# Optimization experiments

Measured on AMD Instinct MI355X. Metric: run time of the kernel, lower is better.

Reference implementation:

```python
import jax, jax.numpy as jnp
import numpy as np

FEATURE_DIM = 128
NUM_EDGES = 640000
NUM_NODES = 40000


def setup_inputs() -> dict:
    key = jax.random.key(0)
    ks = jax.random.split(key, 10)
    d = FEATURE_DIM
    scale = 1.0 / np.sqrt(d)
    inp = {
        "messages": jax.random.normal(ks[0], (NUM_EDGES, d), dtype=jnp.float32),
        "receivers": jax.random.randint(ks[1], (NUM_EDGES,), 0, NUM_NODES, dtype=jnp.int32),
        "num_segments": NUM_NODES,
        "Wk": jax.random.normal(ks[2], (d, d), dtype=jnp.float32) * scale,
        "bk": jnp.zeros((d,), dtype=jnp.float32),
        "Wv": jax.random.normal(ks[3], (d, d), dtype=jnp.float32) * scale,
        "bv": jnp.zeros((d,), dtype=jnp.float32),
        "Wq": jax.random.normal(ks[4], (d, d), dtype=jnp.float32) * scale,
        "bq": jnp.zeros((d,), dtype=jnp.float32),
        "Wo": jax.random.normal(ks[5], (d, d), dtype=jnp.float32) * scale,
        "bo": jnp.zeros((d,), dtype=jnp.float32),
    }
    return inp


def reference(messages, receivers, num_segments, Wk, bk, Wv, bv, Wq, bq, Wo, bo):
    d = messages.shape[-1]
    # per-edge key/value projections
    keys = messages @ Wk + bk            # [E, d]
    values = messages @ Wv + bv          # [E, d]
    # node-level summed messages -> queries
    summed = jax.ops.segment_sum(messages, receivers, num_segments)  # [N, d]
    queries = summed @ Wq + bq                                       # [N, d]
    # scalar attention score per edge (dot over full feature dim)
    msg_q = queries[receivers]                                       # [E, d]
    scores = jnp.sum(msg_q * keys, axis=-1) / jnp.sqrt(jnp.float32(d))  # [E]
    # segment softmax over edges sharing a receiver
    max_s = jax.ops.segment_max(scores, receivers, num_segments)     # [N]
    exp_s = jnp.exp(scores - max_s[receivers])                       # [E]
    sum_e = jax.ops.segment_sum(exp_s, receivers, num_segments)      # [N]
    attn = exp_s / (sum_e[receivers] + 1e-08)                        # [E]
    # weighted scatter-sum of values, then output projection
    agg = jax.ops.segment_sum(values * attn[:, None], receivers, num_segments)  # [N, d]
    return agg @ Wo + bo
```

## Files before the change

### kernel.cpp

```cpp
#include <hip/hip_runtime.h>
#include <hip/hip_bf16.h>

#define D 128
#define RSQRT_D 0.088388347648318440550f


__global__ void hist_kernel(const int* __restrict__ recv, int* __restrict__ cnt, int E) {
    int e = blockIdx.x * blockDim.x + threadIdx.x;
    if (e >= E) return;
    atomicAdd(&cnt[recv[e]], 1);
}

#define SCAN_B 256
__global__ void scan1_kernel(const int* __restrict__ cnt, int* __restrict__ excl,
                             int* __restrict__ bsum, int N) {
    __shared__ int tmp[SCAN_B];
    int i = blockIdx.x * SCAN_B + threadIdx.x;
    int v = (i < N) ? cnt[i] : 0;
    tmp[threadIdx.x] = v;
    __syncthreads();
#pragma unroll
    for (int off = 1; off < SCAN_B; off <<= 1) {
        int t = (threadIdx.x >= off) ? tmp[threadIdx.x - off] : 0;
        __syncthreads();
        tmp[threadIdx.x] += t;
        __syncthreads();
    }
    if (i < N) excl[i] = tmp[threadIdx.x] - v;
    if (threadIdx.x == SCAN_B - 1) bsum[blockIdx.x] = tmp[threadIdx.x];
}

__global__ void scan2_kernel(int* __restrict__ bsum, int nb) {
    __shared__ int tmp[SCAN_B];
    int v = (threadIdx.x < nb) ? bsum[threadIdx.x] : 0;
    tmp[threadIdx.x] = v;
    __syncthreads();
#pragma unroll
    for (int off = 1; off < SCAN_B; off <<= 1) {
        int t = (threadIdx.x >= off) ? tmp[threadIdx.x - off] : 0;
        __syncthreads();
        tmp[threadIdx.x] += t;
        __syncthreads();
    }
    if (threadIdx.x < nb) bsum[threadIdx.x] = tmp[threadIdx.x] - v;
}

__global__ void scan3_kernel(const int* __restrict__ excl, const int* __restrict__ bsum,
                             int* __restrict__ start, int N, int E) {
    int i = blockIdx.x * SCAN_B + threadIdx.x;
    if (i < N) start[i] = excl[i] + bsum[blockIdx.x];
    if (i == N) start[N] = E;
}

__global__ void fill_kernel(const int* __restrict__ recv, const int* __restrict__ start,
                            int* __restrict__ cursor, int* __restrict__ eidx, int E) {
    int e = blockIdx.x * blockDim.x + threadIdx.x;
    if (e >= E) return;
    int r = recv[e];
    int p = atomicAdd(&cursor[r], 1);
    eidx[start[r] + p] = e;
}


__global__ void fold_wvo_kernel(const float* __restrict__ Wv, const float* __restrict__ Wo,
                                const float* __restrict__ bv,
                                float* __restrict__ Wvo, float* __restrict__ bvo) {
    int j = threadIdx.x;
    int i = blockIdx.x;
    if (i < D) {
        float acc = 0.f;
        for (int k = 0; k < D; ++k) acc += Wv[(size_t)i * D + k] * Wo[(size_t)k * D + j];
        Wvo[(size_t)i * D + j] = acc;
    } else {
        float acc = 0.f;
        for (int k = 0; k < D; ++k) acc += bv[k] * Wo[(size_t)k * D + j];
        bvo[j] = acc;
    }
}

__global__ void fold_wqk_kernel(const float* __restrict__ Wq, const float* __restrict__ Wk,
                                const float* __restrict__ bq, const float* __restrict__ bk,
                                float* __restrict__ Wqk, float* __restrict__ bqk,
                                float* __restrict__ wqb, float* __restrict__ bqb) {
    int j = threadIdx.x;
    int i = blockIdx.x;
    if (i < D) {
        float acc = 0.f;
        for (int t = 0; t < D; ++t) acc += Wq[(size_t)i * D + t] * Wk[(size_t)j * D + t];
        Wqk[(size_t)i * D + j] = acc;
    } else if (i == D) {
        float acc = 0.f;
        for (int t = 0; t < D; ++t) acc += bq[t] * Wk[(size_t)j * D + t];
        bqk[j] = acc;
    } else {
        float acc = 0.f;
        for (int t = 0; t < D; ++t) acc += Wq[(size_t)j * D + t] * bk[t];
        wqb[j] = acc;
        if (j == 0) {
            float b = 0.f;
            for (int t = 0; t < D; ++t) b += bq[t] * bk[t];
            *bqb = b;
        }
    }
}


__global__ __launch_bounds__(256) void nodesum_kernel(
        const float* __restrict__ msg, const int* __restrict__ eidx,
        const int* __restrict__ start, float* __restrict__ summed, int N) {
    int wave = threadIdx.x >> 6;
    int lane = threadIdx.x & 63;
    int n = blockIdx.x * 4 + wave;
    if (n >= N) return;
    int s0 = start[n], s1 = start[n + 1];
    float2 acc = make_float2(0.f, 0.f);
    for (int j = s0; j < s1; ++j) {
        int e = eidx[j];
        float2 mm = ((const float2*)(msg + (size_t)e * D))[lane];
        acc.x += mm.x;
        acc.y += mm.y;
    }
    ((float2*)(summed + (size_t)n * D))[lane] = acc;
}

__global__ __launch_bounds__(256) void attn_kernel(
        const float* __restrict__ msg, const int* __restrict__ eidx,
        const int* __restrict__ start, const float* __restrict__ qk,
        const float* __restrict__ qb, float* __restrict__ S,
        float* __restrict__ sumexp, int N) {
    int wave = threadIdx.x >> 6;
    int lane = threadIdx.x & 63;
    int n = blockIdx.x * 4 + wave;
    if (n >= N) return;
    int s0 = start[n], s1 = start[n + 1];
    float2 q = ((const float2*)(qk + (size_t)n * D))[lane];
    float qbn = qb[n];
    float m = -3.4e38f, ssum = 0.f;
    float2 acc = make_float2(0.f, 0.f);

    float2 cur;
    if (s0 < s1) {
        int e0 = eidx[s0];
        cur = ((const float2*)(msg + (size_t)e0 * D))[lane];
    }
    for (int j = s0; j < s1; ++j) {
        float2 nxt;
        if (j + 1 < s1) {
            int e1 = eidx[j + 1];
            nxt = ((const float2*)(msg + (size_t)e1 * D))[lane];
        }
        float p = cur.x * q.x + cur.y * q.y;
#pragma unroll
        for (int off = 1; off < 64; off <<= 1) p += __shfl_xor(p, off);
        float sc = (p + qbn) * RSQRT_D;
        float nm = fmaxf(m, sc);
        float scale = __expf(m - nm);
        float ee = __expf(sc - nm);
        ssum = ssum * scale + ee;
        acc.x = acc.x * scale + ee * cur.x;
        acc.y = acc.y * scale + ee * cur.y;
        m = nm;
        cur = nxt;
    }
    float w = 1.f / (ssum + 1e-8f);
    ((float2*)(S + (size_t)n * D))[lane] = make_float2(acc.x * w, acc.y * w);
    if (lane == 0) sumexp[n] = ssum;
}


#define GN 32
__global__ __launch_bounds__(256) void gemm128_kernel(
        const float* __restrict__ A, const float* __restrict__ B,
        float* __restrict__ C,
        const float* __restrict__ bias,
        const float* __restrict__ sumexp,
        const float* __restrict__ bvec,
        int N) {
    __shared__ float Bs[D * D];
    __shared__ float As[GN * D];
    int t = threadIdx.x;
    const float4* Bg4 = (const float4*)B;
    float4* Bs4 = (float4*)Bs;
#pragma unroll
    for (int k = 0; k < 16; ++k) Bs4[t + 256 * k] = Bg4[t + 256 * k];
    int n0 = blockIdx.x * GN;
    const float4* Ag4 = (const float4*)(A + (size_t)n0 * D);
    float4* As4 = (float4*)As;
#pragma unroll
    for (int k = 0; k < 4; ++k) As4[t + 256 * k] = Ag4[t + 256 * k];
    __syncthreads();

    int c = t & 31;
    int slot = t >> 5;
    float4 acc[4];
#pragma unroll
    for (int u = 0; u < 4; ++u) acc[u] = make_float4(0.f, 0.f, 0.f, 0.f);
    const float4* Bsr = (const float4*)Bs;
    for (int i = 0; i < D; i += 4) {
        float4 a[4];
#pragma unroll
        for (int u = 0; u < 4; ++u) a[u] = *(const float4*)(As + (slot + 8 * u) * D + i);
#pragma unroll
        for (int ii = 0; ii < 4; ++ii) {
            float4 b = Bsr[(i + ii) * 32 + c];
#pragma unroll
            for (int u = 0; u < 4; ++u) {
                float av = (ii == 0) ? a[u].x : (ii == 1) ? a[u].y : (ii == 2) ? a[u].z : a[u].w;
                acc[u].x += av * b.x; acc[u].y += av * b.y;
                acc[u].z += av * b.z; acc[u].w += av * b.w;
            }
        }
    }
    float4 bias4 = bias ? ((const float4*)bias)[c] : make_float4(0.f, 0.f, 0.f, 0.f);
    float4 bv4 = bvec ? ((const float4*)bvec)[c] : make_float4(0.f, 0.f, 0.f, 0.f);
#pragma unroll
    for (int u = 0; u < 4; ++u) {
        int n = n0 + slot + 8 * u;
        if (n >= N) continue;
        float4 r = acc[u];
        r.x += bias4.x; r.y += bias4.y; r.z += bias4.z; r.w += bias4.w;
        if (sumexp) {
            float se = sumexp[n];
            float sa = se / (se + 1e-8f);
            r.x += sa * bv4.x; r.y += sa * bv4.y; r.z += sa * bv4.z; r.w += sa * bv4.w;
        }
        ((float4*)(C + (size_t)n * D))[c] = r;
    }
}

__global__ void rowdot_kernel(const float* __restrict__ A, const float* __restrict__ v,
                              const float* __restrict__ addc,
                              float* __restrict__ out, int N) {
    int g = blockIdx.x * blockDim.x + threadIdx.x;
    int lane = g & 63;
    int n = g >> 6;
    if (n >= N) return;
    const float2* a2 = (const float2*)(A + (size_t)n * D);
    const float2* v2 = (const float2*)v;
    float2 a = a2[lane], b = v2[lane];
    float s = a.x * b.x + a.y * b.y;
#pragma unroll
    for (int off = 32; off; off >>= 1) s += __shfl_down(s, off);
    if (lane == 0) out[n] = s + addc[0];
}


extern "C" void kernel_launch(void* const* d_in, const int* in_sizes, int n_in,
                              void* d_out, int out_size, void* d_ws, size_t ws_size,
                              hipStream_t stream) {
    const float* msg = (const float*)d_in[0];
    const int* recv = (const int*)d_in[1];
    const float* Wk = (const float*)d_in[3];
    const float* bk = (const float*)d_in[4];
    const float* Wv = (const float*)d_in[5];
    const float* bv = (const float*)d_in[6];
    const float* Wq = (const float*)d_in[7];
    const float* bq = (const float*)d_in[8];
    const float* Wo = (const float*)d_in[9];
    const float* bo = (const float*)d_in[10];
    float* out = (float*)d_out;

    int E = in_sizes[0] / D;
    int N = out_size / D;

    char* wsb = (char*)d_ws;
    size_t o = 0;
    auto alloc = [&](size_t elems) { void* p = wsb + o; o += elems * 4; return p; };

    int* cnt    = (int*)alloc(N);
    int* cursor = (int*)alloc(N);
    int* start  = (int*)alloc(N + 1);
    int* excl   = (int*)alloc(N);
    int* bsum   = (int*)alloc(SCAN_B);
    int* eidx   = (int*)alloc(E);
    float* summed = (float*)alloc((size_t)N * D);
    float* qk     = (float*)alloc((size_t)N * D);
    float* qb     = (float*)alloc(N);
    float* S      = (float*)alloc((size_t)N * D);
    float* sumexp = (float*)alloc(N);
    float* Wqk    = (float*)alloc(D * D);
    float* bqk    = (float*)alloc(D);
    float* wqb    = (float*)alloc(D);
    float* bqb    = (float*)alloc(1);
    float* Wvo    = (float*)alloc(D * D);
    float* bvo    = (float*)alloc(D);

    hipMemsetAsync(cnt, 0, 2 * (size_t)N * sizeof(int), stream);

    fold_wvo_kernel<<<D + 1, D, 0, stream>>>(Wv, Wo, bv, Wvo, bvo);
    fold_wqk_kernel<<<D + 2, D, 0, stream>>>(Wq, Wk, bq, bk, Wqk, bqk, wqb, bqb);

    int nbE = (E + 255) / 256;
    int nbS = (N + SCAN_B - 1) / SCAN_B;
    hist_kernel<<<nbE, 256, 0, stream>>>(recv, cnt, E);
    scan1_kernel<<<nbS, SCAN_B, 0, stream>>>(cnt, excl, bsum, N);
    scan2_kernel<<<1, SCAN_B, 0, stream>>>(bsum, nbS);
    scan3_kernel<<<(N + 1 + SCAN_B - 1) / SCAN_B, SCAN_B, 0, stream>>>(excl, bsum, start, N, E);
    fill_kernel<<<nbE, 256, 0, stream>>>(recv, start, cursor, eidx, E);

    nodesum_kernel<<<(N + 3) / 4, 256, 0, stream>>>(msg, eidx, start, summed, N);

    gemm128_kernel<<<(N + GN - 1) / GN, 256, 0, stream>>>(summed, Wqk, qk, bqk, nullptr, nullptr, N);
    rowdot_kernel<<<(N * 64 + 255) / 256, 256, 0, stream>>>(summed, wqb, bqb, qb, N);

    attn_kernel<<<(N + 3) / 4, 256, 0, stream>>>(msg, eidx, start, qk, qb, S, sumexp, N);

    gemm128_kernel<<<(N + GN - 1) / GN, 256, 0, stream>>>(S, Wvo, out, bo, sumexp, bvo, N);
}
```

Measured before the change: 763.7 us.

## Fuse node-sum, query GEMM, segment softmax and output GEMM into one kernel

Replaces the nodesum, two GEMM, rowdot and attention kernels with a single per-wave kernel that handles four nodes: it sums their messages, computes the folded query projection with readlane broadcasts against a 2x2-packed weight layout, runs online softmax four edges at a time, and applies the folded output projection in registers. This removes the intermediate N×D buffers and their global round trips, plus several launches. The cost is that the GEMMs now re-read weights from global/L2 per wave rather than from shared memory. The edge loops are also unrolled by four for more loads in flight, which raises register pressure and gives fewer waves overall.

Measured after the change: 1.098 ms. 1.44x slower.

```diff
diff --git a/kernel.cpp b/kernel.cpp
--- a/kernel.cpp
+++ b/kernel.cpp
@@ -1,8 +1,8 @@
 #include <hip/hip_runtime.h>
-#include <hip/hip_bf16.h>
 
 #define D 128
 #define RSQRT_D 0.088388347648318440550f
+#define NEG_HUGE -3.4e38f
 
 
 __global__ void hist_kernel(const int* __restrict__ recv, int* __restrict__ cnt, int E) {
@@ -64,38 +64,38 @@
 
 __global__ void fold_wvo_kernel(const float* __restrict__ Wv, const float* __restrict__ Wo,
                                 const float* __restrict__ bv,
-                                float* __restrict__ Wvo, float* __restrict__ bvo) {
+                                float* __restrict__ Pvo, float* __restrict__ bvo) {
     int j = threadIdx.x;
     int i = blockIdx.x;
     if (i < D) {
         float acc = 0.f;
-        for (int k = 0; k < D; ++k) acc += Wv[(size_t)i * D + k] * Wo[(size_t)k * D + j];
-        Wvo[(size_t)i * D + j] = acc;
+        for (int t = 0; t < D; ++t) acc += Wv[(size_t)i * D + t] * Wo[(size_t)t * D + j];
+        Pvo[(((i >> 1) * 64 + (j >> 1)) << 2) + ((i & 1) << 1) + (j & 1)] = acc;
     } else {
         float acc = 0.f;
-        for (int k = 0; k < D; ++k) acc += bv[k] * Wo[(size_t)k * D + j];
+        for (int t = 0; t < D; ++t) acc += bv[t] * Wo[(size_t)t * D + j];
         bvo[j] = acc;
     }
 }
 
 __global__ void fold_wqk_kernel(const float* __restrict__ Wq, const float* __restrict__ Wk,
                                 const float* __restrict__ bq, const float* __restrict__ bk,
-                                float* __restrict__ Wqk, float* __restrict__ bqk,
+                                float* __restrict__ Pqk, float* __restrict__ bqk,
                                 float* __restrict__ wqb, float* __restrict__ bqb) {
     int j = threadIdx.x;
     int i = blockIdx.x;
     if (i < D) {
         float acc = 0.f;
         for (int t = 0; t < D; ++t) acc += Wq[(size_t)i * D + t] * Wk[(size_t)j * D + t];
-        Wqk[(size_t)i * D + j] = acc;
-    } else if (i == D) {
-        float acc = 0.f;
-        for (int t = 0; t < D; ++t) acc += bq[t] * Wk[(size_t)j * D + t];
-        bqk[j] = acc;
+        Pqk[(((i >> 1) * 64 + (j >> 1)) << 2) + ((i & 1) << 1) + (j & 1)] = acc;
     } else {
-        float acc = 0.f;
-        for (int t = 0; t < D; ++t) acc += Wq[(size_t)j * D + t] * bk[t];
-        wqb[j] = acc;
+        float a1 = 0.f, a2 = 0.f;
+        for (int t = 0; t < D; ++t) {
+            a1 += bq[t] * Wk[(size_t)j * D + t];
+            a2 += Wq[(size_t)j * D + t] * bk[t];
+        }
+        bqk[j] = a1;
+        wqb[j] = a2;
         if (j == 0) {
             float b = 0.f;
             for (int t = 0; t < D; ++t) b += bq[t] * bk[t];
@@ -105,143 +105,158 @@
 }
 
 
-__global__ __launch_bounds__(256) void nodesum_kernel(
+__device__ __forceinline__ float wave_sum(float v) {
+#pragma unroll
+    for (int off = 1; off < 64; off <<= 1) v += __shfl_xor(v, off);
+    return v;
+}
+
+__device__ __forceinline__ float rdlane(float v, int l) {
+    return __uint_as_float(__builtin_amdgcn_readlane(__float_as_uint(v), l));
+}
+
+#define NB 4
+
+__global__ __launch_bounds__(256) void fused_kernel(
         const float* __restrict__ msg, const int* __restrict__ eidx,
-        const int* __restrict__ start, float* __restrict__ summed, int N) {
-    int wave = threadIdx.x >> 6;
+        const int* __restrict__ start,
+        const float* __restrict__ Pqk, const float* __restrict__ bqk,
+        const float* __restrict__ wqb, const float* __restrict__ bqbp,
+        const float* __restrict__ Pvo, const float* __restrict__ bvo,
+        const float* __restrict__ bo,
+        float* __restrict__ out, int N) {
     int lane = threadIdx.x & 63;
-    int n = blockIdx.x * 4 + wave;
-    if (n >= N) return;
-    int s0 = start[n], s1 = start[n + 1];
-    float2 acc = make_float2(0.f, 0.f);
-    for (int j = s0; j < s1; ++j) {
-        int e = eidx[j];
-        float2 mm = ((const float2*)(msg + (size_t)e * D))[lane];
-        acc.x += mm.x;
-        acc.y += mm.y;
-    }
-    ((float2*)(summed + (size_t)n * D))[lane] = acc;
-}
-
-__global__ __launch_bounds__(256) void attn_kernel(
-        const float* __restrict__ msg, const int* __restrict__ eidx,
-        const int* __restrict__ start, const float* __restrict__ qk,
-        const float* __restrict__ qb, float* __restrict__ S,
-        float* __restrict__ sumexp, int N) {
-    int wave = threadIdx.x >> 6;
-    int lane = threadIdx.x & 63;
-    int n = blockIdx.x * 4 + wave;
-    if (n >= N) return;
-    int s0 = start[n], s1 = start[n + 1];
-    float2 q = ((const float2*)(qk + (size_t)n * D))[lane];
-    float qbn = qb[n];
-    float m = -3.4e38f, ssum = 0.f;
-    float2 acc = make_float2(0.f, 0.f);
-
-    float2 cur;
-    if (s0 < s1) {
-        int e0 = eidx[s0];
-        cur = ((const float2*)(msg + (size_t)e0 * D))[lane];
-    }
-    for (int j = s0; j < s1; ++j) {
-        float2 nxt;
-        if (j + 1 < s1) {
-            int e1 = eidx[j + 1];
-            nxt = ((const float2*)(msg + (size_t)e1 * D))[lane];
-        }
-        float p = cur.x * q.x + cur.y * q.y;
-#pragma unroll
-        for (int off = 1; off < 64; off <<= 1) p += __shfl_xor(p, off);
-        float sc = (p + qbn) * RSQRT_D;
-        float nm = fmaxf(m, sc);
-        float scale = __expf(m - nm);
-        float ee = __expf(sc - nm);
-        ssum = ssum * scale + ee;
-        acc.x = acc.x * scale + ee * cur.x;
-        acc.y = acc.y * scale + ee * cur.y;
-        m = nm;
-        cur = nxt;
-    }
-    float w = 1.f / (ssum + 1e-8f);
-    ((float2*)(S + (size_t)n * D))[lane] = make_float2(acc.x * w, acc.y * w);
-    if (lane == 0) sumexp[n] = ssum;
-}
-
-
-#define GN 32
-__global__ __launch_bounds__(256) void gemm128_kernel(
-        const float* __restrict__ A, const float* __restrict__ B,
-        float* __restrict__ C,
-        const float* __restrict__ bias,
-        const float* __restrict__ sumexp,
-        const float* __restrict__ bvec,
-        int N) {
-    __shared__ float Bs[D * D];
-    __shared__ float As[GN * D];
-    int t = threadIdx.x;
-    const float4* Bg4 = (const float4*)B;
-    float4* Bs4 = (float4*)Bs;
-#pragma unroll
-    for (int k = 0; k < 16; ++k) Bs4[t + 256 * k] = Bg4[t + 256 * k];
-    int n0 = blockIdx.x * GN;
-    const float4* Ag4 = (const float4*)(A + (size_t)n0 * D);
-    float4* As4 = (float4*)As;
-#pragma unroll
-    for (int k = 0; k < 4; ++k) As4[t + 256 * k] = Ag4[t + 256 * k];
-    __syncthreads();
-
-    int c = t & 31;
-    int slot = t >> 5;
-    float4 acc[4];
-#pragma unroll
-    for (int u = 0; u < 4; ++u) acc[u] = make_float4(0.f, 0.f, 0.f, 0.f);
-    const float4* Bsr = (const float4*)Bs;
-    for (int i = 0; i < D; i += 4) {
-        float4 a[4];
-#pragma unroll
-        for (int u = 0; u < 4; ++u) a[u] = *(const float4*)(As + (slot + 8 * u) * D + i);
-#pragma unroll
-        for (int ii = 0; ii < 4; ++ii) {
-            float4 b = Bsr[(i + ii) * 32 + c];
-#pragma unroll
-            for (int u = 0; u < 4; ++u) {
-                float av = (ii == 0) ? a[u].x : (ii == 1) ? a[u].y : (ii == 2) ? a[u].z : a[u].w;
-                acc[u].x += av * b.x; acc[u].y += av * b.y;
-                acc[u].z += av * b.z; acc[u].w += av * b.w;
-            }
-        }
-    }
-    float4 bias4 = bias ? ((const float4*)bias)[c] : make_float4(0.f, 0.f, 0.f, 0.f);
-    float4 bv4 = bvec ? ((const float4*)bvec)[c] : make_float4(0.f, 0.f, 0.f, 0.f);
-#pragma unroll
-    for (int u = 0; u < 4; ++u) {
-        int n = n0 + slot + 8 * u;
-        if (n >= N) continue;
-        float4 r = acc[u];
-        r.x += bias4.x; r.y += bias4.y; r.z += bias4.z; r.w += bias4.w;
-        if (sumexp) {
-            float se = sumexp[n];
-            float sa = se / (se + 1e-8f);
-            r.x += sa * bv4.x; r.y += sa * bv4.y; r.z += sa * bv4.z; r.w += sa * bv4.w;
-        }
-        ((float4*)(C + (size_t)n * D))[c] = r;
-    }
-}
-
-__global__ void rowdot_kernel(const float* __restrict__ A, const float* __restrict__ v,
-                              const float* __restrict__ addc,
-                              float* __restrict__ out, int N) {
-    int g = blockIdx.x * blockDim.x + threadIdx.x;
-    int lane = g & 63;
-    int n = g >> 6;
-    if (n >= N) return;
-    const float2* a2 = (const float2*)(A + (size_t)n * D);
-    const float2* v2 = (const float2*)v;
-    float2 a = a2[lane], b = v2[lane];
-    float s = a.x * b.x + a.y * b.y;
-#pragma unroll
-    for (int off = 32; off; off >>= 1) s += __shfl_down(s, off);
-    if (lane == 0) out[n] = s + addc[0];
+    int wid = blockIdx.x * (blockDim.x >> 6) + (threadIdx.x >> 6);
+    int n0 = wid * NB;
+    if (n0 >= N) return;
+
+    int s0[NB], s1[NB];
+    float2 sum[NB];
+
+#pragma unroll
+    for (int b = 0; b < NB; ++b) {
+        int n = n0 + b;
+        s0[b] = (n < N) ? start[n] : 0;
+        s1[b] = (n < N) ? start[n + 1] : 0;
+        float2 a0 = {0.f, 0.f}, a1 = {0.f, 0.f}, a2 = {0.f, 0.f}, a3 = {0.f, 0.f};
+        int j = s0[b];
+        for (; j + 4 <= s1[b]; j += 4) {
+            int e0 = eidx[j], e1 = eidx[j + 1], e2 = eidx[j + 2], e3 = eidx[j + 3];
+            float2 r0 = ((const float2*)(msg + (size_t)e0 * D))[lane];
+            float2 r1 = ((const float2*)(msg + (size_t)e1 * D))[lane];
+            float2 r2 = ((const float2*)(msg + (size_t)e2 * D))[lane];
+            float2 r3 = ((const float2*)(msg + (size_t)e3 * D))[lane];
+            a0.x += r0.x; a0.y += r0.y;
+            a1.x += r1.x; a1.y += r1.y;
+            a2.x += r2.x; a2.y += r2.y;
+            a3.x += r3.x; a3.y += r3.y;
+        }
+        for (; j < s1[b]; ++j) {
+            int e = eidx[j];
+            float2 r = ((const float2*)(msg + (size_t)e * D))[lane];
+            a0.x += r.x; a0.y += r.y;
+        }
+        sum[b].x = (a0.x + a1.x) + (a2.x + a3.x);
+        sum[b].y = (a0.y + a1.y) + (a2.y + a3.y);
+    }
+
+    float2 wq = ((const float2*)wqb)[lane];
+    float bqb = bqbp[0];
+    float qb[NB];
+#pragma unroll
+    for (int b = 0; b < NB; ++b)
+        qb[b] = wave_sum(sum[b].x * wq.x + sum[b].y * wq.y) + bqb;
+
+    float2 bq2 = ((const float2*)bqk)[lane];
+    float2 qk[NB];
+#pragma unroll
+    for (int b = 0; b < NB; ++b) qk[b] = bq2;
+    const float4* P4 = (const float4*)Pqk;
+#pragma unroll
+    for (int i = 0; i < 64; ++i) {
+        float4 w = P4[i * 64 + lane];
+#pragma unroll
+        for (int b = 0; b < NB; ++b) {
+            float sx = rdlane(sum[b].x, i);
+            float sy = rdlane(sum[b].y, i);
+            qk[b].x += sx * w.x + sy * w.z;
+            qk[b].y += sx * w.y + sy * w.w;
+        }
+    }
+
+    float2 acc[NB];
+    float mm[NB], ss[NB];
+#pragma unroll
+    for (int b = 0; b < NB; ++b) {
+        acc[b] = make_float2(0.f, 0.f);
+        mm[b] = NEG_HUGE;
+        ss[b] = 0.f;
+    }
+#pragma unroll
+    for (int b = 0; b < NB; ++b) {
+        float2 q = qk[b];
+        float qn = qb[b];
+        for (int j = s0[b]; j < s1[b]; j += 4) {
+            int c = s1[b] - j;
+            int e0 = eidx[j];
+            int e1 = (c > 1) ? eidx[j + 1] : e0;
+            int e2 = (c > 2) ? eidx[j + 2] : e0;
+            int e3 = (c > 3) ? eidx[j + 3] : e0;
+            float2 r0 = ((const float2*)(msg + (size_t)e0 * D))[lane];
+            float2 r1 = ((const float2*)(msg + (size_t)e1 * D))[lane];
+            float2 r2 = ((const float2*)(msg + (size_t)e2 * D))[lane];
+            float2 r3 = ((const float2*)(msg + (size_t)e3 * D))[lane];
+            float p0 = wave_sum(r0.x * q.x + r0.y * q.y);
+            float p1 = wave_sum(r1.x * q.x + r1.y * q.y);
+            float p2 = wave_sum(r2.x * q.x + r2.y * q.y);
+            float p3 = wave_sum(r3.x * q.x + r3.y * q.y);
+            float sc0 = (p0 + qn) * RSQRT_D;
+            float sc1 = (c > 1) ? (p1 + qn) * RSQRT_D : NEG_HUGE;
+            float sc2 = (c > 2) ? (p2 + qn) * RSQRT_D : NEG_HUGE;
+            float sc3 = (c > 3) ? (p3 + qn) * RSQRT_D : NEG_HUGE;
+            float bm = fmaxf(fmaxf(sc0, sc1), fmaxf(sc2, sc3));
+            float nm = fmaxf(mm[b], bm);
+            float scale = __expf(mm[b] - nm);
+            float w0 = __expf(sc0 - nm);
+            float w1 = __expf(sc1 - nm);
+            float w2 = __expf(sc2 - nm);
+            float w3 = __expf(sc3 - nm);
+            ss[b] = ss[b] * scale + ((w0 + w1) + (w2 + w3));
+            acc[b].x = acc[b].x * scale + w0 * r0.x + w1 * r1.x + w2 * r2.x + w3 * r3.x;
+            acc[b].y = acc[b].y * scale + w0 * r0.y + w1 * r1.y + w2 * r2.y + w3 * r3.y;
+            mm[b] = nm;
+        }
+    }
+
+    float2 S[NB], o[NB];
+    float2 bo2 = ((const float2*)bo)[lane];
+    float2 bv2 = ((const float2*)bvo)[lane];
+#pragma unroll
+    for (int b = 0; b < NB; ++b) {
+        float inv = 1.f / (ss[b] + 1e-8f);
+        S[b].x = acc[b].x * inv;
+        S[b].y = acc[b].y * inv;
+        float sa = ss[b] * inv;
+        o[b].x = bo2.x + sa * bv2.x;
+        o[b].y = bo2.y + sa * bv2.y;
+    }
+    const float4* V4 = (const float4*)Pvo;
+#pragma unroll
+    for (int i = 0; i < 64; ++i) {
+        float4 w = V4[i * 64 + lane];
+#pragma unroll
+        for (int b = 0; b < NB; ++b) {
+            float sx = rdlane(S[b].x, i);
+            float sy = rdlane(S[b].y, i);
+            o[b].x += sx * w.x + sy * w.z;
+            o[b].y += sx * w.y + sy * w.w;
+        }
+    }
+#pragma unroll
+    for (int b = 0; b < NB; ++b) {
+        int n = n0 + b;
+        if (n < N) ((float2*)(out + (size_t)n * D))[lane] = o[b];
+    }
 }
 
 
@@ -273,22 +288,17 @@
     int* excl   = (int*)alloc(N);
     int* bsum   = (int*)alloc(SCAN_B);
     int* eidx   = (int*)alloc(E);
-    float* summed = (float*)alloc((size_t)N * D);
-    float* qk     = (float*)alloc((size_t)N * D);
-    float* qb     = (float*)alloc(N);
-    float* S      = (float*)alloc((size_t)N * D);
-    float* sumexp = (float*)alloc(N);
-    float* Wqk    = (float*)alloc(D * D);
-    float* bqk    = (float*)alloc(D);
-    float* wqb    = (float*)alloc(D);
-    float* bqb    = (float*)alloc(1);
-    float* Wvo    = (float*)alloc(D * D);
-    float* bvo    = (float*)alloc(D);
+    float* Pqk  = (float*)alloc(D * D);
+    float* bqk  = (float*)alloc(D);
+    float* wqb  = (float*)alloc(D);
+    float* bqb  = (float*)alloc(1);
+    float* Pvo  = (float*)alloc(D * D);
+    float* bvo  = (float*)alloc(D);
 
     hipMemsetAsync(cnt, 0, 2 * (size_t)N * sizeof(int), stream);
 
-    fold_wvo_kernel<<<D + 1, D, 0, stream>>>(Wv, Wo, bv, Wvo, bvo);
-    fold_wqk_kernel<<<D + 2, D, 0, stream>>>(Wq, Wk, bq, bk, Wqk, bqk, wqb, bqb);
+    fold_wvo_kernel<<<D + 1, D, 0, stream>>>(Wv, Wo, bv, Pvo, bvo);
+    fold_wqk_kernel<<<D + 1, D, 0, stream>>>(Wq, Wk, bq, bk, Pqk, bqk, wqb, bqb);
 
     int nbE = (E + 255) / 256;
     int nbS = (N + SCAN_B - 1) / SCAN_B;
@@ -298,12 +308,8 @@
     scan3_kernel<<<(N + 1 + SCAN_B - 1) / SCAN_B, SCAN_B, 0, stream>>>(excl, bsum, start, N, E);
     fill_kernel<<<nbE, 256, 0, stream>>>(recv, start, cursor, eidx, E);
 
-    nodesum_kernel<<<(N + 3) / 4, 256, 0, stream>>>(msg, eidx, start, summed, N);
-
-    gemm128_kernel<<<(N + GN - 1) / GN, 256, 0, stream>>>(summed, Wqk, qk, bqk, nullptr, nullptr, N);
-    rowdot_kernel<<<(N * 64 + 255) / 256, 256, 0, stream>>>(summed, wqb, bqb, qb, N);
-
-    attn_kernel<<<(N + 3) / 4, 256, 0, stream>>>(msg, eidx, start, qk, qb, S, sumexp, N);
-
-    gemm128_kernel<<<(N + GN - 1) / GN, 256, 0, stream>>>(S, Wvo, out, bo, sumexp, bvo, N);
-}
+    int wavesNeeded = (N + NB - 1) / NB;
+    int blocks = (wavesNeeded + 3) / 4;
+    fused_kernel<<<blocks, 256, 0, stream>>>(msg, eidx, start, Pqk, bqk, wqb, bqb,
+                                             Pvo, bvo, bo, out, N);
+}
```
